# Kernel optimization log

Measured on AMD Instinct MI355X. Metric: run time of the kernel, lower is better.

The kernel has to match this reference:

```python
import jax, jax.numpy as jnp
import numpy as np

B = 1024
NIF = 2048   # n_image_features
V = 10000    # vocab_size
E = 512      # embedding_dim
H = 1024     # hidden_size
L = 32       # max_sentence_length
ND = 3       # num distractors


def _lstm_cell(x, h, c, Wih, Whh, bih, bhh):
    # torch LSTMCell: gates ordered i, f, g, o
    g = x @ Wih.T + bih + h @ Whh.T + bhh
    i, f, gc, o = jnp.split(g, 4, axis=-1)
    c = jax.nn.sigmoid(f) * c + jax.nn.sigmoid(i) * jnp.tanh(gc)
    h = jax.nn.sigmoid(o) * jnp.tanh(c)
    return h, c


def setup_inputs() -> dict:
    key = jax.random.key(0)
    ks = jax.random.split(key, 20)
    s = 0.02
    inp = {
        "target": jax.random.normal(ks[0], (B, NIF), jnp.float32),
        "distractors": jax.random.normal(ks[1], (ND, B, NIF), jnp.float32),
        "start_token_idx": 1,
        "max_sentence_length": L,
        # Sender params
        "W_aff": s * jax.random.normal(ks[2], (H, NIF), jnp.float32),
        "b_aff": jnp.zeros((H,), jnp.float32),
        "emb_s": s * jax.random.normal(ks[3], (V, E), jnp.float32),
        "Wih_s": s * jax.random.normal(ks[4], (4 * H, E), jnp.float32),
        "Whh_s": s * jax.random.normal(ks[5], (4 * H, H), jnp.float32),
        "bih_s": jnp.zeros((4 * H,), jnp.float32),
        "bhh_s": jnp.zeros((4 * H,), jnp.float32),
        "Wp": s * jax.random.normal(ks[6], (V, H), jnp.float32),
        "bp": jnp.zeros((V,), jnp.float32),
        # Receiver params
        "emb_r": s * jax.random.normal(ks[7], (V, E), jnp.float32),
        "Wih_r": s * jax.random.normal(ks[8], (4 * H, E), jnp.float32),
        "Whh_r": s * jax.random.normal(ks[9], (4 * H, H), jnp.float32),
        "bih_r": jnp.zeros((4 * H,), jnp.float32),
        "bhh_r": jnp.zeros((4 * H,), jnp.float32),
        "W_out": s * jax.random.normal(ks[10], (NIF, H), jnp.float32),
        "b_out": jnp.zeros((NIF,), jnp.float32),
    }
    return inp


def reference(target, distractors, start_token_idx, max_sentence_length,
              W_aff, b_aff, emb_s, Wih_s, Whh_s, bih_s, bhh_s, Wp, bp,
              emb_r, Wih_r, Whh_r, bih_r, bhh_r, W_out, b_out):
    Bt = target.shape[0]

    # ---- Sender: greedy decode (eval-mode argmax, matching greedy=True) ----
    h0 = target @ W_aff.T + b_aff
    c0 = jnp.zeros_like(h0)
    w0 = emb_s[jnp.full((Bt,), start_token_idx, dtype=jnp.int32)]

    def send_step(carry, _):
        h, c, w = carry
        h, c = _lstm_cell(w, h, c, Wih_s, Whh_s, bih_s, bhh_s)
        logits = h @ Wp.T + bp                         # [B, V]
        idx = jnp.argmax(logits, axis=-1)              # greedy token
        logp = jnp.take_along_axis(jax.nn.log_softmax(logits, axis=-1),
                                   idx[:, None], axis=-1)[:, 0]
        w = emb_s[idx]
        return (h, c, w), (idx, logp)

    _, (message, logps) = jax.lax.scan(send_step, (h0, c0, w0), None,
                                       length=max_sentence_length)
    message = message.T            # [B, L]
    log_prob = logps[-1]           # log_prob of last sampled word, [B]

    # ---- Receiver: encode message ----
    hr = jnp.zeros((Bt, H), jnp.float32)
    cr = jnp.zeros((Bt, H), jnp.float32)

    def recv_step(carry, w_idx):
        h, c = carry
        h, c = _lstm_cell(emb_r[w_idx], h, c, Wih_r, Whh_r, bih_r, bhh_r)
        return (h, c), None

    (hr, cr), _ = jax.lax.scan(recv_step, (hr, cr), message.T)
    r = hr @ W_out.T + b_out       # [B, NIF]

    # ---- Hinge loss over distractors ----
    r_T = r.T                                       # [NIF, B]
    t_r = target @ r_T                              # [B, B]
    d_r = jnp.einsum('nbf,fc->nbc', distractors, r_T)  # [ND, B, B]
    loss = jnp.sum(jnp.maximum(0.0, 1.0 - t_r[None] + d_r), axis=0)  # [B, B]
    loss = -loss * log_prob        # broadcast [B] over last dim, as in torch
    return jnp.mean(loss)
```

## Files before the change

### kernel.cpp

```cpp
#include <hip/hip_runtime.h>
#include <hip/hip_bf16.h>
#include <cstdint>
#include <cstddef>

#define Bc   1024
#define NIFc 2048
#define Vc   10000
#define Ec   512
#define Hc   1024
#define Lc   32
#define NDc  3
#define G4c  4096
#define NTv  79
#define TMLD 80
#define XLD  3584
#define XOFF 512

typedef __attribute__((ext_vector_type(4))) float f32x4;
typedef __attribute__((ext_vector_type(8))) short s16x8;
typedef __attribute__((ext_vector_type(4))) short s16x4;

#define GBM 128
#define GBN 128
#define GBK 64

__device__ __forceinline__ void gld_lds16(void* lds, const void* g) {
    __builtin_amdgcn_global_load_lds(
        (const __attribute__((address_space(1))) unsigned int*)g,
        (__attribute__((address_space(3))) unsigned int*)lds,
        16, 0, 0);
}

template<int OBF>
__device__ __forceinline__ void gemm_body(
    const __hip_bfloat16* __restrict__ A, int lda,
    const __hip_bfloat16* __restrict__ W, int ldw,
    const float* __restrict__ bias, void* __restrict__ Cv,
    int M, int N, int K, int bx, int by,
    float* __restrict__ tile_max, int tmld)
{
    __shared__ __align__(16) __hip_bfloat16 As[GBM * GBK];
    __shared__ __align__(16) __hip_bfloat16 Ws[GBN * GBK];
    __shared__ float smax[GBM];

    const int tid  = threadIdx.x;
    const int lane = tid & 63;
    const int wave = tid >> 6;
    const int m0 = by * GBM;
    const int n0 = bx * GBN;

    const __hip_bfloat16* ag[4];
    const __hip_bfloat16* wg[4];
    #pragma unroll
    for (int r = 0; r < 4; ++r) {
        int p = r * 256 + tid;
        int m = p >> 3;
        int q = (p & 7) ^ (m & 7);
        int am = m0 + m; if (am >= M) am = M - 1;
        ag[r] = A + (size_t)am * lda + q * 8;
        int wn = n0 + m; if (wn >= N) wn = N - 1;
        wg[r] = W + (size_t)wn * ldw + q * 8;
    }

    f32x4 acc[4][4];
    #pragma unroll
    for (int i = 0; i < 4; ++i)
        #pragma unroll
        for (int j = 0; j < 4; ++j)
            acc[i][j] = (f32x4)(0.0f);

    const int hm = (wave & 1) << 6;
    const int hn = (wave >> 1) << 6;
    const int lm = lane & 15;
    const int quad = lane >> 4;

    const int nk = K >> 6;
    for (int kt = 0; kt < nk; ++kt) {
        __syncthreads();
        #pragma unroll
        for (int r = 0; r < 4; ++r) {
            int ldsbase = (r * 256 + wave * 64) * 8;
            gld_lds16(As + ldsbase, ag[r]);
            gld_lds16(Ws + ldsbase, wg[r]);
            ag[r] += GBK;
            wg[r] += GBK;
        }
        __syncthreads();
        #pragma unroll
        for (int c = 0; c < 2; ++c) {
            s16x8 af[4], wf[4];
            int q = c * 4 + quad;
            #pragma unroll
            for (int i = 0; i < 4; ++i) {
                int m = hm + i * 16 + lm;
                af[i] = *(const s16x8*)(As + ((m << 3) + (q ^ (m & 7))) * 8);
                int n = hn + i * 16 + lm;
                wf[i] = *(const s16x8*)(Ws + ((n << 3) + (q ^ (n & 7))) * 8);
            }
            #pragma unroll
            for (int i = 0; i < 4; ++i)
                #pragma unroll
                for (int j = 0; j < 4; ++j)
                    acc[i][j] = __builtin_amdgcn_mfma_f32_16x16x32_bf16(
                        af[i], wf[j], acc[i][j], 0, 0, 0);
        }
    }

    float rowmax[4][4];
    #pragma unroll
    for (int i = 0; i < 4; ++i)
        #pragma unroll
        for (int rr = 0; rr < 4; ++rr)
            rowmax[i][rr] = -__builtin_inff();

    #pragma unroll
    for (int i = 0; i < 4; ++i) {
        int mbase = m0 + hm + i * 16 + quad * 4;
        #pragma unroll
        for (int j = 0; j < 4; ++j) {
            int n = n0 + hn + j * 16 + lm;
            if (n < N) {
                float bv = bias ? bias[n] : 0.0f;
                #pragma unroll
                for (int rr = 0; rr < 4; ++rr) {
                    float v = acc[i][j][rr] + bv;
                    if (mbase + rr < M) {
                        if (OBF)
                            ((__hip_bfloat16*)Cv)[(size_t)(mbase + rr) * N + n] =
                                __float2bfloat16(v);
                        else
                            ((float*)Cv)[(size_t)(mbase + rr) * N + n] = v;
                    }
                    rowmax[i][rr] = fmaxf(rowmax[i][rr], v);
                }
            }
        }
    }

    if (tile_max) {
        #pragma unroll
        for (int i = 0; i < 4; ++i)
            #pragma unroll
            for (int rr = 0; rr < 4; ++rr) {
                float v = rowmax[i][rr];
                v = fmaxf(v, __shfl_xor(v, 1));
                v = fmaxf(v, __shfl_xor(v, 2));
                v = fmaxf(v, __shfl_xor(v, 4));
                v = fmaxf(v, __shfl_xor(v, 8));
                rowmax[i][rr] = v;
            }
        __syncthreads();
        if (hn == 0 && lm == 0) {
            #pragma unroll
            for (int i = 0; i < 4; ++i)
                #pragma unroll
                for (int rr = 0; rr < 4; ++rr)
                    smax[hm + i * 16 + quad * 4 + rr] = rowmax[i][rr];
        }
        __syncthreads();
        if (hn == 64 && lm == 0) {
            #pragma unroll
            for (int i = 0; i < 4; ++i)
                #pragma unroll
                for (int rr = 0; rr < 4; ++rr) {
                    int r = hm + i * 16 + quad * 4 + rr;
                    smax[r] = fmaxf(smax[r], rowmax[i][rr]);
                }
        }
        __syncthreads();
        if (tid < GBM)
            tile_max[(size_t)(m0 + tid) * tmld + bx] = smax[tid];
    }
}

__global__ __launch_bounds__(256) void gemm_bf16_tn(
    const __hip_bfloat16* __restrict__ A, int lda,
    const __hip_bfloat16* __restrict__ W, int ldw,
    const float* __restrict__ bias, float* __restrict__ C,
    int M, int N, int K, float* __restrict__ tile_max, int tmld)
{
    gemm_body<0>(A, lda, W, ldw, bias, C, M, N, K, blockIdx.x, blockIdx.y,
                 tile_max, tmld);
}

__global__ __launch_bounds__(256) void gemm_bf16_obf(
    const __hip_bfloat16* __restrict__ A, int lda,
    const __hip_bfloat16* __restrict__ W, int ldw,
    __hip_bfloat16* __restrict__ C, int M, int N, int K)
{
    gemm_body<1>(A, lda, W, ldw, nullptr, C, M, N, K, blockIdx.x, blockIdx.y,
                 nullptr, 0);
}

__global__ __launch_bounds__(256) void gemm_bf16_sk2(
    const __hip_bfloat16* __restrict__ A, int lda,
    const __hip_bfloat16* __restrict__ W, int ldw,
    float* __restrict__ Cpart, int M, int N, int Ksub)
{
    int z = blockIdx.z;
    gemm_body<0>(A + (size_t)z * Ksub, lda, W + (size_t)z * Ksub, ldw, nullptr,
                 Cpart + (size_t)z * M * N, M, N, Ksub, blockIdx.x, blockIdx.y,
                 nullptr, 0);
}

__global__ __launch_bounds__(256) void split3_a_kernel(
    const float* __restrict__ in, int ldin,
    __hip_bfloat16* __restrict__ out, int ldo, int coff, int M, int K)
{
    int i = blockIdx.x * 256 + threadIdx.x;
    if (i >= M * K) return;
    int m = i / K, k = i - m * K;
    float v = in[(size_t)m * ldin + k];
    __hip_bfloat16 hi = __float2bfloat16(v);
    float lo = v - __bfloat162float(hi);
    __hip_bfloat16* row = out + (size_t)m * ldo + coff;
    row[k] = hi;
    row[K + k] = __float2bfloat16(lo);
    row[2 * K + k] = hi;
}

__global__ __launch_bounds__(256) void split3_w_kernel(
    const float* __restrict__ in, int ldin,
    __hip_bfloat16* __restrict__ out, int ldo, int coff, int M, int K)
{
    int i = blockIdx.x * 256 + threadIdx.x;
    if (i >= M * K) return;
    int m = i / K, k = i - m * K;
    float v = in[(size_t)m * ldin + k];
    __hip_bfloat16 hi = __float2bfloat16(v);
    float lo = v - __bfloat162float(hi);
    __hip_bfloat16* row = out + (size_t)m * ldo + coff;
    row[k] = hi;
    row[K + k] = hi;
    row[2 * K + k] = __float2bfloat16(lo);
}

__global__ __launch_bounds__(256) void cast2d_kernel(
    const float* __restrict__ in, int ldin,
    __hip_bfloat16* __restrict__ out, int ldo, int coff, int M, int K)
{
    int i = blockIdx.x * 256 + threadIdx.x;
    if (i >= M * K) return;
    int m = i / K, k = i - m * K;
    out[(size_t)m * ldo + coff + k] = __float2bfloat16(in[(size_t)m * ldin + k]);
}

__global__ __launch_bounds__(256) void gather_cast_kernel(
    const float* __restrict__ emb, int E, const int* __restrict__ idx,
    int stride, __hip_bfloat16* __restrict__ out, int ldo, int coff, int Brows)
{
    int i = blockIdx.x * 256 + threadIdx.x;
    if (i >= Brows * E) return;
    int b = i / E, k = i - b * E;
    out[(size_t)b * ldo + coff + k] =
        __float2bfloat16(emb[(size_t)idx[(size_t)b * stride] * E + k]);
}

__global__ __launch_bounds__(256) void add_vec_kernel(
    const float* __restrict__ a, const float* __restrict__ b,
    float* __restrict__ o, int n)
{
    int i = blockIdx.x * 256 + threadIdx.x;
    if (i < n) o[i] = a[i] + b[i];
}

__device__ __forceinline__ short bf16bits(float x) {
    __hip_bfloat16 t = __float2bfloat16(x);
    return *reinterpret_cast<short*>(&t);
}

__device__ __forceinline__ float b16f(short s) {
    return __bfloat162float(*reinterpret_cast<__hip_bfloat16*>(&s));
}

__global__ __launch_bounds__(256) void lstm_fused_s(
    const float* __restrict__ gp0, const float* __restrict__ gp1,
    const float* __restrict__ bias, float* __restrict__ h,
    float* __restrict__ c, __hip_bfloat16* __restrict__ h3x,
    const __hip_bfloat16* __restrict__ xg, const int* __restrict__ tok,
    int tstride)
{
    int i = blockIdx.x * 256 + threadIdx.x;
    if (i >= Bc * Hc / 4) return;
    int b = i >> 8;
    int j = (i & 255) * 4;
    size_t g0 = (size_t)b * G4c + j;
    f32x4 gi = *(const f32x4*)(gp0 + g0) + *(const f32x4*)(gp1 + g0)
             + *(const f32x4*)(bias + j);
    f32x4 gf = *(const f32x4*)(gp0 + g0 + Hc) + *(const f32x4*)(gp1 + g0 + Hc)
             + *(const f32x4*)(bias + Hc + j);
    f32x4 gg = *(const f32x4*)(gp0 + g0 + 2 * Hc) + *(const f32x4*)(gp1 + g0 + 2 * Hc)
             + *(const f32x4*)(bias + 2 * Hc + j);
    f32x4 go = *(const f32x4*)(gp0 + g0 + 3 * Hc) + *(const f32x4*)(gp1 + g0 + 3 * Hc)
             + *(const f32x4*)(bias + 3 * Hc + j);
    if (xg) {
        const __hip_bfloat16* xr = xg + (size_t)tok[(size_t)b * tstride] * G4c;
        s16x4 xi = *(const s16x4*)(xr + j);
        s16x4 xf = *(const s16x4*)(xr + Hc + j);
        s16x4 xc = *(const s16x4*)(xr + 2 * Hc + j);
        s16x4 xo = *(const s16x4*)(xr + 3 * Hc + j);
        #pragma unroll
        for (int k = 0; k < 4; ++k) {
            gi[k] += b16f(xi[k]);
            gf[k] += b16f(xf[k]);
            gg[k] += b16f(xc[k]);
            go[k] += b16f(xo[k]);
        }
    }
    size_t hix = (size_t)b * Hc + j;
    f32x4 cv = *(const f32x4*)(c + hix);
    f32x4 cn, hv;
    s16x4 hi4, lo4;
    #pragma unroll
    for (int k = 0; k < 4; ++k) {
        float si = 1.0f / (1.0f + expf(-gi[k]));
        float sf = 1.0f / (1.0f + expf(-gf[k]));
        float so = 1.0f / (1.0f + expf(-go[k]));
        float cc = sf * cv[k] + si * tanhf(gg[k]);
        cn[k] = cc;
        float hh = so * tanhf(cc);
        hv[k] = hh;
        hi4[k] = bf16bits(hh);
        lo4[k] = bf16bits(hh - __bfloat162float(__float2bfloat16(hh)));
    }
    *(f32x4*)(c + hix) = cn;
    *(f32x4*)(h + hix) = hv;
    __hip_bfloat16* row = h3x + (size_t)b * XLD + XOFF;
    *(s16x4*)(row + j) = hi4;
    *(s16x4*)(row + Hc + j) = lo4;
    *(s16x4*)(row + 2 * Hc + j) = hi4;
}

__global__ __launch_bounds__(256) void combine_h0_kernel(
    const float* __restrict__ p0, const float* __restrict__ p1,
    const float* __restrict__ bias, float* __restrict__ h,
    __hip_bfloat16* __restrict__ h3x)
{
    int i = blockIdx.x * 256 + threadIdx.x;
    if (i >= Bc * Hc / 4) return;
    int b = i >> 8;
    int j = (i & 255) * 4;
    size_t ix = (size_t)b * Hc + j;
    f32x4 v = *(const f32x4*)(p0 + ix) + *(const f32x4*)(p1 + ix)
            + *(const f32x4*)(bias + j);
    *(f32x4*)(h + ix) = v;
    s16x4 hi4, lo4;
    #pragma unroll
    for (int k = 0; k < 4; ++k) {
        hi4[k] = bf16bits(v[k]);
        lo4[k] = bf16bits(v[k] - __bfloat162float(__float2bfloat16(v[k])));
    }
    __hip_bfloat16* row = h3x + (size_t)b * XLD + XOFF;
    *(s16x4*)(row + j) = hi4;
    *(s16x4*)(row + Hc + j) = lo4;
    *(s16x4*)(row + 2 * Hc + j) = hi4;
}

__global__ __launch_bounds__(256) void lstm_fused_r(
    const float* __restrict__ gp0, const float* __restrict__ gp1,
    const float* __restrict__ bias, float* __restrict__ h,
    float* __restrict__ c, __hip_bfloat16* __restrict__ xh_r,
    const __hip_bfloat16* __restrict__ xg, const int* __restrict__ tok,
    int has_g, const float* __restrict__ emb, const int* __restrict__ msg_next)
{
    int i = blockIdx.x * 256 + threadIdx.x;
    if (i >= Bc * Hc / 4) return;
    int b = i >> 8;
    int j = (i & 255) * 4;
    f32x4 gi = *(const f32x4*)(bias + j);
    f32x4 gf = *(const f32x4*)(bias + Hc + j);
    f32x4 gg = *(const f32x4*)(bias + 2 * Hc + j);
    f32x4 go = *(const f32x4*)(bias + 3 * Hc + j);
    if (has_g) {
        size_t g0 = (size_t)b * G4c + j;
        gi += *(const f32x4*)(gp0 + g0) + *(const f32x4*)(gp1 + g0);
        gf += *(const f32x4*)(gp0 + g0 + Hc) + *(const f32x4*)(gp1 + g0 + Hc);
        gg += *(const f32x4*)(gp0 + g0 + 2 * Hc) + *(const f32x4*)(gp1 + g0 + 2 * Hc);
        go += *(const f32x4*)(gp0 + g0 + 3 * Hc) + *(const f32x4*)(gp1 + g0 + 3 * Hc);
    }
    if (xg) {
        const __hip_bfloat16* xr = xg + (size_t)tok[b] * G4c;
        s16x4 xi = *(const s16x4*)(xr + j);
        s16x4 xf = *(const s16x4*)(xr + Hc + j);
        s16x4 xc = *(const s16x4*)(xr + 2 * Hc + j);
        s16x4 xo = *(const s16x4*)(xr + 3 * Hc + j);
        #pragma unroll
        for (int k = 0; k < 4; ++k) {
            gi[k] += b16f(xi[k]);
            gf[k] += b16f(xf[k]);
            gg[k] += b16f(xc[k]);
            go[k] += b16f(xo[k]);
        }
    }
    size_t hix = (size_t)b * Hc + j;
    f32x4 cv = *(const f32x4*)(c + hix);
    f32x4 cn, hv;
    s16x4 hb4;
    #pragma unroll
    for (int k = 0; k < 4; ++k) {
        float si = 1.0f / (1.0f + expf(-gi[k]));
        float sf = 1.0f / (1.0f + expf(-gf[k]));
        float so = 1.0f / (1.0f + expf(-go[k]));
        float cc = sf * cv[k] + si * tanhf(gg[k]);
        cn[k] = cc;
        float hh = so * tanhf(cc);
        hv[k] = hh;
        hb4[k] = bf16bits(hh);
    }
    *(f32x4*)(c + hix) = cn;
    *(f32x4*)(h + hix) = hv;
    *(s16x4*)(xh_r + (size_t)b * 1536 + Ec + j) = hb4;
    if (!xg && msg_next && j < Ec) {
        int t2 = msg_next[b];
        f32x4 e = *(const f32x4*)(emb + (size_t)t2 * Ec + j);
        s16x4 eb;
        #pragma unroll
        for (int k = 0; k < 4; ++k) eb[k] = bf16bits(e[k]);
        *(s16x4*)(xh_r + (size_t)b * 1536 + j) = eb;
    }
}

__global__ __launch_bounds__(256) void argmax_rescore_v3(
    const float* __restrict__ logits, const float* __restrict__ tmax,
    const float* __restrict__ h, const float* __restrict__ Wp,
    const float* __restrict__ bp, const float* __restrict__ emb,
    int* __restrict__ msg_t, float* __restrict__ logp,
    __hip_bfloat16* __restrict__ xdst, int want_logp)
{
    const int b = blockIdx.x;
    const int tid = threadIdx.x;
    const int lane = tid & 63;
    const int wave = tid >> 6;
    const float* row = logits + (size_t)b * Vc;

    __shared__ float stm[128];
    __shared__ float redm[256];
    __shared__ float reds[256];
    __shared__ int   qt[32];
    __shared__ int   nq, cnt;
    __shared__ int   cand[64];
    __shared__ float score[64];
    __shared__ float sbestv;
    __shared__ int   sbestj;

    float tv = (tid < NTv) ? tmax[(size_t)b * TMLD + tid] : -__builtin_inff();
    if (tid < 128) stm[tid] = tv;
    redm[tid] = tv;
    reds[tid] = (tid < NTv) ? tv : 0.0f;
    if (tid == 0) { nq = 0; cnt = 0; }
    __syncthreads();
    #pragma unroll
    for (int s = 128; s > 0; s >>= 1) {
        if (tid < s) {
            redm[tid] = fmaxf(redm[tid], redm[tid + s]);
            reds[tid] += reds[tid + s];
        }
        __syncthreads();
    }
    const float m = redm[0];
    const float spread = m - reds[0] * (1.0f / NTv);
    const float delta = 0.08f * spread + 1e-6f * (1.0f + fabsf(m));

    if (tid < NTv && stm[tid] >= m - delta) {
        int k = atomicAdd(&nq, 1);
        if (k < 32) qt[k] = tid;
    }
    __syncthreads();
    int nqt = nq < 32 ? nq : 32;

    for (int qi = 0; qi < nqt; qi += 2) {
        int ti = qi + (tid >> 7);
        if (ti < nqt) {
            int j = qt[ti] * 128 + (tid & 127);
            if (j < Vc) {
                float v = row[j];
                if (v >= m - delta) {
                    int k = atomicAdd(&cnt, 1);
                    if (k < 64) cand[k] = j;
                }
            }
        }
    }
    __syncthreads();
    int nc = cnt < 64 ? cnt : 64;

    const float* hrow = h + (size_t)b * Hc;
    for (int cix = wave; cix < nc; cix += 4) {
        int j = cand[cix];
        const float* wrow = Wp + (size_t)j * Hc;
        float part = 0.0f;
        #pragma unroll
        for (int kk = 0; kk < 4; ++kk) {
            int k = kk * 256 + lane * 4;
            f32x4 hv = *(const f32x4*)(hrow + k);
            f32x4 wv = *(const f32x4*)(wrow + k);
            part = fmaf(hv.x, wv.x, part);
            part = fmaf(hv.y, wv.y, part);
            part = fmaf(hv.z, wv.z, part);
            part = fmaf(hv.w, wv.w, part);
        }
        #pragma unroll
        for (int off = 1; off < 64; off <<= 1)
            part += __shfl_xor(part, off);
        if (lane == 0) score[cix] = part + bp[j];
    }
    __syncthreads();
    if (tid == 0) {
        float bv = -__builtin_inff();
        int bj = 0x7fffffff;
        for (int cix = 0; cix < nc; ++cix) {
            float v = score[cix];
            int j = cand[cix];
            if (v > bv || (v == bv && j < bj)) { bv = v; bj = j; }
        }
        sbestv = bv;
        sbestj = bj;
        msg_t[b] = bj;
    }
    __syncthreads();
    const int bestj = sbestj;

    if (want_logp) {
        float s = 0.0f;
        const f32x4* row4 = (const f32x4*)row;
        for (int j = tid; j < Vc / 4; j += 256) {
            f32x4 v = row4[j];
            s += expf(v.x - m) + expf(v.y - m) + expf(v.z - m) + expf(v.w - m);
        }
        redm[tid] = s;
        __syncthreads();
        #pragma unroll
        for (int st = 128; st > 0; st >>= 1) {
            if (tid < st) redm[tid] += redm[tid + st];
            __syncthreads();
        }
        if (tid == 0) logp[b] = sbestv - (m + logf(redm[0]));
    }

    if (xdst && tid < 128) {
        int k = tid * 4;
        f32x4 e = *(const f32x4*)(emb + (size_t)bestj * Ec + k);
        s16x4 h4;
        #pragma unroll
        for (int kk = 0; kk < 4; ++kk) h4[kk] = bf16bits(e[kk]);
        *(s16x4*)(xdst + (size_t)b * XLD + k) = h4;
    }
}

__global__ __launch_bounds__(256) void hinge_kernel(
    const float* __restrict__ S, const float* __restrict__ logp,
    float* __restrict__ partials, int Bn)
{
    int tid = threadIdx.x;
    int n = Bn * Bn;
    float acc = 0.0f;
    for (int idx = blockIdx.x * 256 + tid; idx < n; idx += gridDim.x * 256) {
        int j = idx & (Bn - 1);
        float s0 = S[idx];
        float l = fmaxf(0.0f, 1.0f - s0 + S[n + idx])
                + fmaxf(0.0f, 1.0f - s0 + S[2 * n + idx])
                + fmaxf(0.0f, 1.0f - s0 + S[3 * n + idx]);
        acc += l * logp[j];
    }
    __shared__ float sv[256];
    sv[tid] = acc;
    __syncthreads();
    for (int s = 128; s > 0; s >>= 1) {
        if (tid < s) sv[tid] += sv[tid + s];
        __syncthreads();
    }
    if (tid == 0) partials[blockIdx.x] = sv[0];
}

__global__ __launch_bounds__(256) void final_reduce_kernel(
    const float* __restrict__ partials, int np, float* __restrict__ out,
    float scale)
{
    int tid = threadIdx.x;
    float acc = 0.0f;
    for (int i = tid; i < np; i += 256) acc += partials[i];
    __shared__ float sv[256];
    sv[tid] = acc;
    __syncthreads();
    for (int s = 128; s > 0; s >>= 1) {
        if (tid < s) sv[tid] += sv[tid + s];
        __syncthreads();
    }
    if (tid == 0) out[0] = sv[0] * scale;
}

extern "C" void kernel_launch(void* const* d_in, const int* in_sizes, int n_in,
                              void* d_out, int out_size, void* d_ws, size_t ws_size,
                              hipStream_t stream)
{
    (void)in_sizes; (void)n_in; (void)out_size;

    const float* target  = (const float*)d_in[0];
    const float* distr   = (const float*)d_in[1];
    const int*   start_t = (const int*)d_in[2];
    const float* W_aff = (const float*)d_in[4];
    const float* b_aff = (const float*)d_in[5];
    const float* emb_s = (const float*)d_in[6];
    const float* Wih_s = (const float*)d_in[7];
    const float* Whh_s = (const float*)d_in[8];
    const float* bih_s = (const float*)d_in[9];
    const float* bhh_s = (const float*)d_in[10];
    const float* Wp    = (const float*)d_in[11];
    const float* bp    = (const float*)d_in[12];
    const float* emb_r = (const float*)d_in[13];
    const float* Wih_r = (const float*)d_in[14];
    const float* Whh_r = (const float*)d_in[15];
    const float* bih_r = (const float*)d_in[16];
    const float* bhh_r = (const float*)d_in[17];
    const float* W_out = (const float*)d_in[18];
    const float* b_out = (const float*)d_in[19];

    dim3 blk(256);

    char* b0 = (char*)d_ws;
    size_t off = 0;
    auto take = [&](size_t bytes) -> char* {
        char* p = b0 + off;
        off += (bytes + 511) & ~(size_t)511;
        return p;
    };
    const size_t MB = 1024 * 1024;
    __hip_bfloat16* W3x     = (__hip_bfloat16*)take((size_t)G4c * XLD * 2);
    __hip_bfloat16* Wp_b    = (__hip_bfloat16*)take((size_t)Vc * Hc * 2);
    __hip_bfloat16* WihWhh_r= (__hip_bfloat16*)take((size_t)G4c * 1536 * 2);
    __hip_bfloat16* W_out_b = (__hip_bfloat16*)take((size_t)NIFc * Hc * 2);
    __hip_bfloat16* h3x     = (__hip_bfloat16*)take((size_t)Bc * XLD * 2);
    __hip_bfloat16* xh_r    = (__hip_bfloat16*)take((size_t)Bc * 1536 * 2);
    float* gates_p = (float*)take((size_t)2 * Bc * G4c * 4);
    float* h_s    = (float*)take((size_t)Bc * Hc * 4);
    float* c_s    = (float*)take((size_t)Bc * Hc * 4);
    float* hr     = (float*)take((size_t)Bc * Hc * 4);
    float* cr     = (float*)take((size_t)Bc * Hc * 4);
    float* logp   = (float*)take(Bc * 4);
    int*   msg    = (int*)take((size_t)Lc * Bc * 4);
    float* parts  = (float*)take(1024 * 4);
    float* bias_s = (float*)take(G4c * 4);
    float* bias_r = (float*)take(G4c * 4);
    float* tilemax= (float*)take((size_t)Bc * TMLD * 4);
    char*  U      = take(48 * MB);

    __hip_bfloat16* Xg_s = (__hip_bfloat16*)take((size_t)Vc * G4c * 2);
    const int use_tab_s = (off <= ws_size);
    __hip_bfloat16* Xg_r = (__hip_bfloat16*)take((size_t)Vc * G4c * 2);
    const int use_tab_r = (off <= ws_size);

    __hip_bfloat16* target3 = (__hip_bfloat16*)U;
    __hip_bfloat16* W_aff3  = (__hip_bfloat16*)(U + 13 * MB);
    __hip_bfloat16* emb_b   = (__hip_bfloat16*)(U + 26 * MB);
    float*          logits  = (float*)U;
    __hip_bfloat16* A4b     = (__hip_bfloat16*)U;
    float*          r_f     = (float*)(U + 17 * MB);
    __hip_bfloat16* r_b     = (__hip_bfloat16*)(U + 26 * MB);
    float*          S       = (float*)(U + 31 * MB);

    cast2d_kernel<<<(G4c * Ec + 255) / 256, blk, 0, stream>>>(
        Wih_s, Ec, W3x, XLD, 0, G4c, Ec);
    split3_w_kernel<<<(G4c * Hc + 255) / 256, blk, 0, stream>>>(
        Whh_s, Hc, W3x, XLD, XOFF, G4c, Hc);
    cast2d_kernel<<<(Vc * Hc + 255) / 256, blk, 0, stream>>>(
        Wp, Hc, Wp_b, Hc, 0, Vc, Hc);
    split3_a_kernel<<<(Bc * NIFc + 255) / 256, blk, 0, stream>>>(
        target, NIFc, target3, 6144, 0, Bc, NIFc);
    split3_w_kernel<<<(Hc * NIFc + 255) / 256, blk, 0, stream>>>(
        W_aff, NIFc, W_aff3, 6144, 0, Hc, NIFc);
    cast2d_kernel<<<(G4c * Ec + 255) / 256, blk, 0, stream>>>(
        Wih_r, Ec, WihWhh_r, 1536, 0, G4c, Ec);
    cast2d_kernel<<<(G4c * Hc + 255) / 256, blk, 0, stream>>>(
        Whh_r, Hc, WihWhh_r, 1536, Ec, G4c, Hc);
    cast2d_kernel<<<(NIFc * Hc + 255) / 256, blk, 0, stream>>>(
        W_out, Hc, W_out_b, Hc, 0, NIFc, Hc);
    add_vec_kernel<<<(G4c + 255) / 256, blk, 0, stream>>>(bih_s, bhh_s,
                                                          bias_s, G4c);
    add_vec_kernel<<<(G4c + 255) / 256, blk, 0, stream>>>(bih_r, bhh_r,
                                                          bias_r, G4c);

    if (use_tab_s) {
        cast2d_kernel<<<(Vc * Ec + 255) / 256, blk, 0, stream>>>(
            emb_s, Ec, emb_b, Ec, 0, Vc, Ec);
        gemm_bf16_obf<<<dim3(G4c / GBN, (Vc + GBM - 1) / GBM), blk, 0, stream>>>(
            emb_b, Ec, W3x, XLD, Xg_s, Vc, G4c, Ec);
    }
    if (use_tab_r) {
        cast2d_kernel<<<(Vc * Ec + 255) / 256, blk, 0, stream>>>(
            emb_r, Ec, emb_b, Ec, 0, Vc, Ec);
        gemm_bf16_obf<<<dim3(G4c / GBN, (Vc + GBM - 1) / GBM), blk, 0, stream>>>(
            emb_b, Ec, WihWhh_r, 1536, Xg_r, Vc, G4c, Ec);
    }

    gemm_bf16_sk2<<<dim3(Hc / GBN, Bc / GBM, 2), blk, 0, stream>>>(
        target3, 6144, W_aff3, 6144, gates_p, Bc, Hc, 3072);
    combine_h0_kernel<<<(Bc * Hc / 4 + 255) / 256, blk, 0, stream>>>(
        gates_p, gates_p + (size_t)Bc * Hc, b_aff, h_s, h3x);
    hipMemsetAsync(c_s, 0, (size_t)Bc * Hc * 4, stream);
    if (!use_tab_s)
        gather_cast_kernel<<<(Bc * Ec + 255) / 256, blk, 0, stream>>>(
            emb_s, Ec, start_t, 0, h3x, XLD, 0, Bc);

    for (int t = 0; t < Lc; ++t) {
        if (use_tab_s) {
            gemm_bf16_sk2<<<dim3(G4c / GBN, Bc / GBM, 2), blk, 0, stream>>>(
                h3x + XOFF, XLD, W3x + XOFF, XLD, gates_p, Bc, G4c, 1536);
            lstm_fused_s<<<(Bc * Hc / 4 + 255) / 256, blk, 0, stream>>>(
                gates_p, gates_p + (size_t)Bc * G4c, bias_s, h_s, c_s, h3x,
                Xg_s, (t == 0) ? start_t : (msg + (t - 1) * Bc),
                (t == 0) ? 0 : 1);
        } else {
            gemm_bf16_sk2<<<dim3(G4c / GBN, Bc / GBM, 2), blk, 0, stream>>>(
                h3x, XLD, W3x, XLD, gates_p, Bc, G4c, 1792);
            lstm_fused_s<<<(Bc * Hc / 4 + 255) / 256, blk, 0, stream>>>(
                gates_p, gates_p + (size_t)Bc * G4c, bias_s, h_s, c_s, h3x,
                nullptr, nullptr, 0);
        }
        gemm_bf16_tn<<<dim3((Vc + GBN - 1) / GBN, Bc / GBM), blk, 0, stream>>>(
            h3x + XOFF, XLD, Wp_b, Hc, bp, logits, Bc, Vc, Hc, tilemax, TMLD);
        argmax_rescore_v3<<<Bc, blk, 0, stream>>>(
            logits, tilemax, h_s, Wp, bp, emb_s, msg + t * Bc, logp,
            (!use_tab_s && t < Lc - 1) ? h3x : nullptr, (t == Lc - 1) ? 1 : 0);
    }

    hipMemsetAsync(hr, 0, (size_t)Bc * Hc * 4, stream);
    hipMemsetAsync(cr, 0, (size_t)Bc * Hc * 4, stream);
    hipMemsetAsync(xh_r, 0, (size_t)Bc * 1536 * 2, stream);
    if (!use_tab_r)
        gather_cast_kernel<<<(Bc * Ec + 255) / 256, blk, 0, stream>>>(
            emb_r, Ec, msg, 1, xh_r, 1536, 0, Bc);
    for (int t = 0; t < Lc; ++t) {
        if (use_tab_r) {
            if (t > 0)
                gemm_bf16_sk2<<<dim3(G4c / GBN, Bc / GBM, 2), blk, 0, stream>>>(
                    xh_r + Ec, 1536, WihWhh_r + Ec, 1536, gates_p, Bc, G4c, 512);
            lstm_fused_r<<<(Bc * Hc / 4 + 255) / 256, blk, 0, stream>>>(
                gates_p, gates_p + (size_t)Bc * G4c, bias_r, hr, cr, xh_r,
                Xg_r, msg + t * Bc, (t > 0) ? 1 : 0, nullptr, nullptr);
        } else {
            gemm_bf16_sk2<<<dim3(G4c / GBN, Bc / GBM, 2), blk, 0, stream>>>(
                xh_r, 1536, WihWhh_r, 1536, gates_p, Bc, G4c, 768);
            lstm_fused_r<<<(Bc * Hc / 4 + 255) / 256, blk, 0, stream>>>(
                gates_p, gates_p + (size_t)Bc * G4c, bias_r, hr, cr, xh_r,
                nullptr, nullptr, 1, emb_r,
                (t < Lc - 1) ? (msg + (t + 1) * Bc) : nullptr);
        }
    }

    gemm_bf16_tn<<<dim3(NIFc / GBN, Bc / GBM), blk, 0, stream>>>(
        xh_r + Ec, 1536, W_out_b, Hc, b_out, r_f, Bc, NIFc, Hc, nullptr, 0);

    cast2d_kernel<<<(Bc * NIFc + 255) / 256, blk, 0, stream>>>(
        target, NIFc, A4b, NIFc, 0, Bc, NIFc);
    cast2d_kernel<<<(NDc * Bc * NIFc + 255) / 256, blk, 0, stream>>>(
        distr, NIFc, A4b + (size_t)Bc * NIFc, NIFc, 0, NDc * Bc, NIFc);
    cast2d_kernel<<<(Bc * NIFc + 255) / 256, blk, 0, stream>>>(
        r_f, NIFc, r_b, NIFc, 0, Bc, NIFc);
    gemm_bf16_tn<<<dim3(Bc / GBN, 4 * Bc / GBM), blk, 0, stream>>>(
        A4b, NIFc, r_b, NIFc, nullptr, S, 4 * Bc, Bc, NIFc, nullptr, 0);

    hinge_kernel<<<1024, blk, 0, stream>>>(S, logp, parts, Bc);
    final_reduce_kernel<<<1, blk, 0, stream>>>(
        parts, 1024, (float*)d_out, -1.0f / ((float)Bc * (float)Bc));
}
```

Measured before the change: 4.537 ms.

## Interleave sender and receiver LSTM steps with fused multi-GEMM and argmax-LSTM kernels

When both gate tables fit in the workspace, the sender decode and the receiver encode now run in one loop. Each step issues a single launch that covers the next sender gate GEMM, the vocabulary logits GEMM and the receiver gate GEMM, split by block index. A second fused kernel then does the argmax and rescore, the sender LSTM cell update and the receiver LSTM cell update. This cuts per-step launches and lets independent GEMMs share the GPU, filling more CUs. The cost is larger, branchy kernels and a more complex dependency schedule, with the old path kept as a fallback.

```diff
diff --git a/kernel.cpp b/kernel.cpp
--- a/kernel.cpp
+++ b/kernel.cpp
@@ -24,6 +24,12 @@
 #define GBN 128
 #define GBK 64
 
+struct __align__(16) GemmSmem {
+    __hip_bfloat16 As[GBM * GBK];
+    __hip_bfloat16 Ws[GBN * GBK];
+    float smax[GBM];
+};
+
 __device__ __forceinline__ void gld_lds16(void* lds, const void* g) {
     __builtin_amdgcn_global_load_lds(
         (const __attribute__((address_space(1))) unsigned int*)g,
@@ -33,15 +39,16 @@
 
 template<int OBF>
 __device__ __forceinline__ void gemm_body(
+    GemmSmem& sm,
     const __hip_bfloat16* __restrict__ A, int lda,
     const __hip_bfloat16* __restrict__ W, int ldw,
     const float* __restrict__ bias, void* __restrict__ Cv,
     int M, int N, int K, int bx, int by,
     float* __restrict__ tile_max, int tmld)
 {
-    __shared__ __align__(16) __hip_bfloat16 As[GBM * GBK];
-    __shared__ __align__(16) __hip_bfloat16 Ws[GBN * GBK];
-    __shared__ float smax[GBM];
+    __hip_bfloat16* As = sm.As;
+    __hip_bfloat16* Ws = sm.Ws;
+    float* smax = sm.smax;
 
     const int tid  = threadIdx.x;
     const int lane = tid & 63;
@@ -179,7 +186,8 @@
     const float* __restrict__ bias, float* __restrict__ C,
     int M, int N, int K, float* __restrict__ tile_max, int tmld)
 {
-    gemm_body<0>(A, lda, W, ldw, bias, C, M, N, K, blockIdx.x, blockIdx.y,
+    __shared__ GemmSmem sm;
+    gemm_body<0>(sm, A, lda, W, ldw, bias, C, M, N, K, blockIdx.x, blockIdx.y,
                  tile_max, tmld);
 }
 
@@ -188,8 +196,9 @@
     const __hip_bfloat16* __restrict__ W, int ldw,
     __hip_bfloat16* __restrict__ C, int M, int N, int K)
 {
-    gemm_body<1>(A, lda, W, ldw, nullptr, C, M, N, K, blockIdx.x, blockIdx.y,
-                 nullptr, 0);
+    __shared__ GemmSmem sm;
+    gemm_body<1>(sm, A, lda, W, ldw, nullptr, C, M, N, K, blockIdx.x,
+                 blockIdx.y, nullptr, 0);
 }
 
 __global__ __launch_bounds__(256) void gemm_bf16_sk2(
@@ -197,10 +206,38 @@
     const __hip_bfloat16* __restrict__ W, int ldw,
     float* __restrict__ Cpart, int M, int N, int Ksub)
 {
+    __shared__ GemmSmem sm;
     int z = blockIdx.z;
-    gemm_body<0>(A + (size_t)z * Ksub, lda, W + (size_t)z * Ksub, ldw, nullptr,
-                 Cpart + (size_t)z * M * N, M, N, Ksub, blockIdx.x, blockIdx.y,
-                 nullptr, 0);
+    gemm_body<0>(sm, A + (size_t)z * Ksub, lda, W + (size_t)z * Ksub, ldw,
+                 nullptr, Cpart + (size_t)z * M * N, M, N, Ksub, blockIdx.x,
+                 blockIdx.y, nullptr, 0);
+}
+
+__global__ __launch_bounds__(256) void gemm_fused_step(
+    int nb_g, int nb_l,
+    const __hip_bfloat16* __restrict__ Ag, const __hip_bfloat16* __restrict__ Wg,
+    float* __restrict__ Cg,
+    const __hip_bfloat16* __restrict__ Al, const __hip_bfloat16* __restrict__ Wl,
+    const float* __restrict__ bl, float* __restrict__ Cl,
+    float* __restrict__ tmax,
+    const __hip_bfloat16* __restrict__ Ar, const __hip_bfloat16* __restrict__ Wr,
+    float* __restrict__ Cr)
+{
+    __shared__ GemmSmem sm;
+    int bid = blockIdx.x;
+    if (bid < nb_g) {
+        gemm_body<0>(sm, Ag, XLD, Wg, XLD, nullptr, Cg,
+                     Bc, G4c, 3072, bid & 31, bid >> 5, nullptr, 0);
+    } else if (bid < nb_g + nb_l) {
+        int rem = bid - nb_g;
+        int by = rem / NTv, bx = rem - by * NTv;
+        gemm_body<0>(sm, Al, XLD, Wl, Hc, bl, Cl, Bc, Vc, Hc, bx, by,
+                     tmax, TMLD);
+    } else {
+        int rem = bid - nb_g - nb_l;
+        gemm_body<0>(sm, Ar, 1536, Wr, 1536, nullptr, Cr,
+                     Bc, G4c, Hc, rem & 31, rem >> 5, nullptr, 0);
+    }
 }
 
 __global__ __launch_bounds__(256) void split3_a_kernel(
@@ -544,6 +581,214 @@
         #pragma unroll
         for (int kk = 0; kk < 4; ++kk) h4[kk] = bf16bits(e[kk]);
         *(s16x4*)(xdst + (size_t)b * XLD + k) = h4;
+    }
+}
+
+__global__ __launch_bounds__(256) void argmax_lstm_step(
+    const float* __restrict__ logits, const float* __restrict__ tmax,
+    const float* __restrict__ h, const float* __restrict__ Wp,
+    const float* __restrict__ bp, int* __restrict__ msg_t,
+    float* __restrict__ logp, int want_logp,
+    int do_s, const float* __restrict__ gp0,
+    const float* __restrict__ bias_s, float* __restrict__ h_s,
+    float* __restrict__ c_s, __hip_bfloat16* __restrict__ h3x,
+    const __hip_bfloat16* __restrict__ Xg_s,
+    int has_gr, const float* __restrict__ gr0,
+    const float* __restrict__ bias_r, float* __restrict__ hr,
+    float* __restrict__ cr, __hip_bfloat16* __restrict__ xh_r,
+    const __hip_bfloat16* __restrict__ Xg_r)
+{
+    const int b = blockIdx.x;
+    const int tid = threadIdx.x;
+    const int lane = tid & 63;
+    const int wave = tid >> 6;
+    const float* row = logits + (size_t)b * Vc;
+
+    __shared__ float stm[128];
+    __shared__ float redm[256];
+    __shared__ float reds[256];
+    __shared__ int   qt[32];
+    __shared__ int   nq, cnt;
+    __shared__ int   cand[64];
+    __shared__ float score[64];
+    __shared__ float sbestv;
+    __shared__ int   sbestj;
+
+    float tv = (tid < NTv) ? tmax[(size_t)b * TMLD + tid] : -__builtin_inff();
+    if (tid < 128) stm[tid] = tv;
+    redm[tid] = tv;
+    reds[tid] = (tid < NTv) ? tv : 0.0f;
+    if (tid == 0) { nq = 0; cnt = 0; }
+    __syncthreads();
+    #pragma unroll
+    for (int s = 128; s > 0; s >>= 1) {
+        if (tid < s) {
+            redm[tid] = fmaxf(redm[tid], redm[tid + s]);
+            reds[tid] += reds[tid + s];
+        }
+        __syncthreads();
+    }
+    const float m = redm[0];
+    const float spread = m - reds[0] * (1.0f / NTv);
+    const float delta = 0.08f * spread + 1e-6f * (1.0f + fabsf(m));
+
+    if (tid < NTv && stm[tid] >= m - delta) {
+        int k = atomicAdd(&nq, 1);
+        if (k < 32) qt[k] = tid;
+    }
+    __syncthreads();
+    int nqt = nq < 32 ? nq : 32;
+
+    for (int qi = 0; qi < nqt; qi += 2) {
+        int ti = qi + (tid >> 7);
+        if (ti < nqt) {
+            int j = qt[ti] * 128 + (tid & 127);
+            if (j < Vc) {
+                float v = row[j];
+                if (v >= m - delta) {
+                    int k = atomicAdd(&cnt, 1);
+                    if (k < 64) cand[k] = j;
+                }
+            }
+        }
+    }
+    __syncthreads();
+    int nc = cnt < 64 ? cnt : 64;
+
+    const float* hrow = h + (size_t)b * Hc;
+    for (int cix = wave; cix < nc; cix += 4) {
+        int j = cand[cix];
+        const float* wrow = Wp + (size_t)j * Hc;
+        float part = 0.0f;
+        #pragma unroll
+        for (int kk = 0; kk < 4; ++kk) {
+            int k = kk * 256 + lane * 4;
+            f32x4 hv = *(const f32x4*)(hrow + k);
+            f32x4 wv = *(const f32x4*)(wrow + k);
+            part = fmaf(hv.x, wv.x, part);
+            part = fmaf(hv.y, wv.y, part);
+            part = fmaf(hv.z, wv.z, part);
+            part = fmaf(hv.w, wv.w, part);
+        }
+        #pragma unroll
+        for (int off = 1; off < 64; off <<= 1)
+            part += __shfl_xor(part, off);
+        if (lane == 0) score[cix] = part + bp[j];
+    }
+    __syncthreads();
+    if (tid == 0) {
+        float bv = -__builtin_inff();
+        int bj = 0x7fffffff;
+        for (int cix = 0; cix < nc; ++cix) {
+            float v = score[cix];
+            int j = cand[cix];
+            if (v > bv || (v == bv && j < bj)) { bv = v; bj = j; }
+        }
+        sbestv = bv;
+        sbestj = bj;
+        msg_t[b] = bj;
+    }
+    __syncthreads();
+    const int tok = sbestj;
+
+    if (want_logp) {
+        float s = 0.0f;
+        const f32x4* row4 = (const f32x4*)row;
+        for (int j = tid; j < Vc / 4; j += 256) {
+            f32x4 v = row4[j];
+            s += expf(v.x - m) + expf(v.y - m) + expf(v.z - m) + expf(v.w - m);
+        }
+        redm[tid] = s;
+        __syncthreads();
+        #pragma unroll
+        for (int st = 128; st > 0; st >>= 1) {
+            if (tid < st) redm[tid] += redm[tid + st];
+            __syncthreads();
+        }
+        if (tid == 0) logp[b] = sbestv - (m + logf(redm[0]));
+        __syncthreads();
+    }
+
+    const int j = tid * 4;
+
+    if (do_s) {
+        size_t g0 = (size_t)b * G4c + j;
+        f32x4 gi = *(const f32x4*)(gp0 + g0) + *(const f32x4*)(bias_s + j);
+        f32x4 gf = *(const f32x4*)(gp0 + g0 + Hc) + *(const f32x4*)(bias_s + Hc + j);
+        f32x4 gg = *(const f32x4*)(gp0 + g0 + 2 * Hc) + *(const f32x4*)(bias_s + 2 * Hc + j);
+        f32x4 go = *(const f32x4*)(gp0 + g0 + 3 * Hc) + *(const f32x4*)(bias_s + 3 * Hc + j);
+        const __hip_bfloat16* xr = Xg_s + (size_t)tok * G4c;
+        s16x4 xi = *(const s16x4*)(xr + j);
+        s16x4 xf = *(const s16x4*)(xr + Hc + j);
+        s16x4 xc = *(const s16x4*)(xr + 2 * Hc + j);
+        s16x4 xo = *(const s16x4*)(xr + 3 * Hc + j);
+        size_t hix = (size_t)b * Hc + j;
+        f32x4 cv = *(const f32x4*)(c_s + hix);
+        f32x4 cn, hv;
+        s16x4 hi4, lo4;
+        #pragma unroll
+        for (int k = 0; k < 4; ++k) {
+            float gik = gi[k] + b16f(xi[k]);
+            float gfk = gf[k] + b16f(xf[k]);
+            float ggk = gg[k] + b16f(xc[k]);
+            float gok = go[k] + b16f(xo[k]);
+            float si = 1.0f / (1.0f + expf(-gik));
+            float sf = 1.0f / (1.0f + expf(-gfk));
+            float so = 1.0f / (1.0f + expf(-gok));
+            float cc = sf * cv[k] + si * tanhf(ggk);
+            cn[k] = cc;
+            float hh = so * tanhf(cc);
+            hv[k] = hh;
+            hi4[k] = bf16bits(hh);
+            lo4[k] = bf16bits(hh - __bfloat162float(__float2bfloat16(hh)));
+        }
+        *(f32x4*)(c_s + hix) = cn;
+        *(f32x4*)(h_s + hix) = hv;
+        __hip_bfloat16* orow = h3x + (size_t)b * XLD + XOFF;
+        *(s16x4*)(orow + j) = hi4;
+        *(s16x4*)(orow + Hc + j) = lo4;
+        *(s16x4*)(orow + 2 * Hc + j) = hi4;
+    }
+
+    {
+        f32x4 gi = *(const f32x4*)(bias_r + j);
+        f32x4 gf = *(const f32x4*)(bias_r + Hc + j);
+        f32x4 gg = *(const f32x4*)(bias_r + 2 * Hc + j);
+        f32x4 go = *(const f32x4*)(bias_r + 3 * Hc + j);
+        if (has_gr) {
+            size_t g0 = (size_t)b * G4c + j;
+            gi += *(const f32x4*)(gr0 + g0);
+            gf += *(const f32x4*)(gr0 + g0 + Hc);
+            gg += *(const f32x4*)(gr0 + g0 + 2 * Hc);
+            go += *(const f32x4*)(gr0 + g0 + 3 * Hc);
+        }
+        const __hip_bfloat16* xr = Xg_r + (size_t)tok * G4c;
+        s16x4 xi = *(const s16x4*)(xr + j);
+        s16x4 xf = *(const s16x4*)(xr + Hc + j);
+        s16x4 xc = *(const s16x4*)(xr + 2 * Hc + j);
+        s16x4 xo = *(const s16x4*)(xr + 3 * Hc + j);
+        size_t hix = (size_t)b * Hc + j;
+        f32x4 cv = *(const f32x4*)(cr + hix);
+        f32x4 cn, hv;
+        s16x4 hb4;
+        #pragma unroll
+        for (int k = 0; k < 4; ++k) {
+            float gik = gi[k] + b16f(xi[k]);
+            float gfk = gf[k] + b16f(xf[k]);
+            float ggk = gg[k] + b16f(xc[k]);
+            float gok = go[k] + b16f(xo[k]);
+            float si = 1.0f / (1.0f + expf(-gik));
+            float sf = 1.0f / (1.0f + expf(-gfk));
+            float so = 1.0f / (1.0f + expf(-gok));
+            float cc = sf * cv[k] + si * tanhf(ggk);
+            cn[k] = cc;
+            float hh = so * tanhf(cc);
+            hv[k] = hh;
+            hb4[k] = bf16bits(hh);
+        }
+        *(f32x4*)(cr + hix) = cn;
+        *(f32x4*)(hr + hix) = hv;
+        *(s16x4*)(xh_r + (size_t)b * 1536 + Ec + j) = hb4;
     }
 }
 
@@ -648,6 +893,7 @@
     const int use_tab_s = (off <= ws_size);
     __hip_bfloat16* Xg_r = (__hip_bfloat16*)take((size_t)Vc * G4c * 2);
     const int use_tab_r = (off <= ws_size);
+    const int use_merged = use_tab_s && use_tab_r;
 
     __hip_bfloat16* target3 = (__hip_bfloat16*)U;
     __hip_bfloat16* W_aff3  = (__hip_bfloat16*)(U + 13 * MB);
@@ -697,53 +943,83 @@
     combine_h0_kernel<<<(Bc * Hc / 4 + 255) / 256, blk, 0, stream>>>(
         gates_p, gates_p + (size_t)Bc * Hc, b_aff, h_s, h3x);
     hipMemsetAsync(c_s, 0, (size_t)Bc * Hc * 4, stream);
-    if (!use_tab_s)
-        gather_cast_kernel<<<(Bc * Ec + 255) / 256, blk, 0, stream>>>(
-            emb_s, Ec, start_t, 0, h3x, XLD, 0, Bc);
-
-    for (int t = 0; t < Lc; ++t) {
-        if (use_tab_s) {
-            gemm_bf16_sk2<<<dim3(G4c / GBN, Bc / GBM, 2), blk, 0, stream>>>(
-                h3x + XOFF, XLD, W3x + XOFF, XLD, gates_p, Bc, G4c, 1536);
-            lstm_fused_s<<<(Bc * Hc / 4 + 255) / 256, blk, 0, stream>>>(
-                gates_p, gates_p + (size_t)Bc * G4c, bias_s, h_s, c_s, h3x,
-                Xg_s, (t == 0) ? start_t : (msg + (t - 1) * Bc),
-                (t == 0) ? 0 : 1);
-        } else {
-            gemm_bf16_sk2<<<dim3(G4c / GBN, Bc / GBM, 2), blk, 0, stream>>>(
-                h3x, XLD, W3x, XLD, gates_p, Bc, G4c, 1792);
-            lstm_fused_s<<<(Bc * Hc / 4 + 255) / 256, blk, 0, stream>>>(
-                gates_p, gates_p + (size_t)Bc * G4c, bias_s, h_s, c_s, h3x,
-                nullptr, nullptr, 0);
-        }
-        gemm_bf16_tn<<<dim3((Vc + GBN - 1) / GBN, Bc / GBM), blk, 0, stream>>>(
-            h3x + XOFF, XLD, Wp_b, Hc, bp, logits, Bc, Vc, Hc, tilemax, TMLD);
-        argmax_rescore_v3<<<Bc, blk, 0, stream>>>(
-            logits, tilemax, h_s, Wp, bp, emb_s, msg + t * Bc, logp,
-            (!use_tab_s && t < Lc - 1) ? h3x : nullptr, (t == Lc - 1) ? 1 : 0);
-    }
-
-    hipMemsetAsync(hr, 0, (size_t)Bc * Hc * 4, stream);
-    hipMemsetAsync(cr, 0, (size_t)Bc * Hc * 4, stream);
-    hipMemsetAsync(xh_r, 0, (size_t)Bc * 1536 * 2, stream);
-    if (!use_tab_r)
-        gather_cast_kernel<<<(Bc * Ec + 255) / 256, blk, 0, stream>>>(
-            emb_r, Ec, msg, 1, xh_r, 1536, 0, Bc);
-    for (int t = 0; t < Lc; ++t) {
-        if (use_tab_r) {
-            if (t > 0)
+
+    if (use_merged) {
+        hipMemsetAsync(cr, 0, (size_t)Bc * Hc * 4, stream);
+
+        gemm_bf16_sk2<<<dim3(G4c / GBN, Bc / GBM, 2), blk, 0, stream>>>(
+            h3x + XOFF, XLD, W3x + XOFF, XLD, gates_p, Bc, G4c, 1536);
+        lstm_fused_s<<<(Bc * Hc / 4 + 255) / 256, blk, 0, stream>>>(
+            gates_p, gates_p + (size_t)Bc * G4c, bias_s, h_s, c_s, h3x,
+            Xg_s, start_t, 0);
+
+        float* gates_s = gates_p;
+        float* gates_r = gates_p + (size_t)Bc * G4c;
+
+        for (int t = 0; t < Lc; ++t) {
+            const int nb_g = (t < Lc - 1) ? 256 : 0;
+            const int nb_r = (t >= 1) ? 256 : 0;
+            gemm_fused_step<<<nb_g + 632 + nb_r, blk, 0, stream>>>(
+                nb_g, 632,
+                h3x + XOFF, W3x + XOFF, gates_s,
+                h3x + XOFF, Wp_b, bp, logits, tilemax,
+                xh_r + Ec, WihWhh_r + Ec, gates_r);
+            argmax_lstm_step<<<Bc, blk, 0, stream>>>(
+                logits, tilemax, h_s, Wp, bp, msg + t * Bc, logp,
+                (t == Lc - 1) ? 1 : 0,
+                (t < Lc - 1) ? 1 : 0, gates_s, bias_s, h_s, c_s, h3x, Xg_s,
+                (t >= 1) ? 1 : 0, gates_r, bias_r, hr, cr, xh_r, Xg_r);
+        }
+    } else {
+        if (!use_tab_s)
+            gather_cast_kernel<<<(Bc * Ec + 255) / 256, blk, 0, stream>>>(
+                emb_s, Ec, start_t, 0, h3x, XLD, 0, Bc);
+
+        for (int t = 0; t < Lc; ++t) {
+            if (use_tab_s) {
                 gemm_bf16_sk2<<<dim3(G4c / GBN, Bc / GBM, 2), blk, 0, stream>>>(
-                    xh_r + Ec, 1536, WihWhh_r + Ec, 1536, gates_p, Bc, G4c, 512);
-            lstm_fused_r<<<(Bc * Hc / 4 + 255) / 256, blk, 0, stream>>>(
-                gates_p, gates_p + (size_t)Bc * G4c, bias_r, hr, cr, xh_r,
-                Xg_r, msg + t * Bc, (t > 0) ? 1 : 0, nullptr, nullptr);
-        } else {
-            gemm_bf16_sk2<<<dim3(G4c / GBN, Bc / GBM, 2), blk, 0, stream>>>(
-                xh_r, 1536, WihWhh_r, 1536, gates_p, Bc, G4c, 768);
-            lstm_fused_r<<<(Bc * Hc / 4 + 255) / 256, blk, 0, stream>>>(
-                gates_p, gates_p + (size_t)Bc * G4c, bias_r, hr, cr, xh_r,
-                nullptr, nullptr, 1, emb_r,
-                (t < Lc - 1) ? (msg + (t + 1) * Bc) : nullptr);
+                    h3x + XOFF, XLD, W3x + XOFF, XLD, gates_p, Bc, G4c, 1536);
+                lstm_fused_s<<<(Bc * Hc / 4 + 255) / 256, blk, 0, stream>>>(
+                    gates_p, gates_p + (size_t)Bc * G4c, bias_s, h_s, c_s, h3x,
+                    Xg_s, (t == 0) ? start_t : (msg + (t - 1) * Bc),
+                    (t == 0) ? 0 : 1);
+            } else {
+                gemm_bf16_sk2<<<dim3(G4c / GBN, Bc / GBM, 2), blk, 0, stream>>>(
+                    h3x, XLD, W3x, XLD, gates_p, Bc, G4c, 1792);
+                lstm_fused_s<<<(Bc * Hc / 4 + 255) / 256, blk, 0, stream>>>(
+                    gates_p, gates_p + (size_t)Bc * G4c, bias_s, h_s, c_s, h3x,
+                    nullptr, nullptr, 0);
+            }
+            gemm_bf16_tn<<<dim3((Vc + GBN - 1) / GBN, Bc / GBM), blk, 0, stream>>>(
+                h3x + XOFF, XLD, Wp_b, Hc, bp, logits, Bc, Vc, Hc, tilemax, TMLD);
+            argmax_rescore_v3<<<Bc, blk, 0, stream>>>(
+                logits, tilemax, h_s, Wp, bp, emb_s, msg + t * Bc, logp,
+                (!use_tab_s && t < Lc - 1) ? h3x : nullptr,
+                (t == Lc - 1) ? 1 : 0);
+        }
+
+        hipMemsetAsync(hr, 0, (size_t)Bc * Hc * 4, stream);
+        hipMemsetAsync(cr, 0, (size_t)Bc * Hc * 4, stream);
+        hipMemsetAsync(xh_r, 0, (size_t)Bc * 1536 * 2, stream);
+        if (!use_tab_r)
+            gather_cast_kernel<<<(Bc * Ec + 255) / 256, blk, 0, stream>>>(
+                emb_r, Ec, msg, 1, xh_r, 1536, 0, Bc);
+        for (int t = 0; t < Lc; ++t) {
+            if (use_tab_r) {
+                if (t > 0)
+                    gemm_bf16_sk2<<<dim3(G4c / GBN, Bc / GBM, 2), blk, 0, stream>>>(
+                        xh_r + Ec, 1536, WihWhh_r + Ec, 1536, gates_p, Bc, G4c, 512);
+                lstm_fused_r<<<(Bc * Hc / 4 + 255) / 256, blk, 0, stream>>>(
+                    gates_p, gates_p + (size_t)Bc * G4c, bias_r, hr, cr, xh_r,
+                    Xg_r, msg + t * Bc, (t > 0) ? 1 : 0, nullptr, nullptr);
+            } else {
+                gemm_bf16_sk2<<<dim3(G4c / GBN, Bc / GBM, 2), blk, 0, stream>>>(
+                    xh_r, 1536, WihWhh_r, 1536, gates_p, Bc, G4c, 768);
+                lstm_fused_r<<<(Bc * Hc / 4 + 255) / 256, blk, 0, stream>>>(
+                    gates_p, gates_p + (size_t)Bc * G4c, bias_r, hr, cr, xh_r,
+                    nullptr, nullptr, 1, emb_r,
+                    (t < Lc - 1) ? (msg + (t + 1) * Bc) : nullptr);
+            }
         }
     }
 
```

Measured after the change: 4.510 ms. No clear change (-0.6%).
